# Kernel optimization log

Measured on AMD Instinct MI355X. Metric: run time of the kernel, lower is better.

The kernel has to match this reference:

```python
import jax, jax.numpy as jnp
import numpy as np

B, T, C, H = 16, 512, 1080, 20  # batch, seq, embd, heads; head_dim = C // H = 54

def setup_inputs() -> dict:
    key = jax.random.key(0)
    k1, k2, k3, k4, k5 = jax.random.split(key, 5)
    s = 0.02
    return {
        "x": jax.random.normal(k1, (B, T, C), dtype=jnp.float32),
        "W_attn": jax.random.normal(k2, (C, 3 * C), dtype=jnp.float32) * s,
        "b_attn": jax.random.normal(k3, (3 * C,), dtype=jnp.float32) * s,
        "W_proj": jax.random.normal(k4, (C, C), dtype=jnp.float32) * s,
        "b_proj": jax.random.normal(k5, (C,), dtype=jnp.float32) * s,
    }

def reference(x, W_attn, b_attn, W_proj, b_proj):
    Bb, Tt, Cc = x.shape
    hd = Cc // H
    qkv = jnp.einsum('btc,cd->btd', x, W_attn) + b_attn  # [B,T,3C]
    q, k, v = jnp.split(qkv, 3, axis=2)
    # [B,T,C] -> [B,H,T,hd]
    q = q.reshape(Bb, Tt, H, hd).transpose(0, 2, 1, 3)
    k = k.reshape(Bb, Tt, H, hd).transpose(0, 2, 1, 3)
    v = v.reshape(Bb, Tt, H, hd).transpose(0, 2, 1, 3)
    att = jnp.einsum('bhqd,bhkd->bhqk', q, k) * (1.0 / jnp.sqrt(jnp.float32(hd)))
    causal = jnp.tril(jnp.ones((Tt, Tt), dtype=bool))
    att = jnp.where(causal, att, -jnp.inf)
    att = jax.nn.softmax(att, axis=-1)
    y = jnp.einsum('bhqk,bhkd->bhqd', att, v)  # [B,H,T,hd]
    y = y.transpose(0, 2, 1, 3).reshape(Bb, Tt, Cc)
    return jnp.einsum('btc,cd->btd', y, W_proj) + b_proj
```

## Files before the change

### kernel.cpp

```cpp
#include <hip/hip_runtime.h>
#include <hip/hip_bf16.h>

#define B_   16
#define T_   512
#define C_   1080
#define H_   20
#define HD_  54
#define DP_  64
#define M_   (B_ * T_)
#define KP_  1088
#define NT_  17
#define NQKV_ 3840
#define NPRJ_ 1152
#define NBT_ (B_ * H_ * T_)

typedef short bf16x8 __attribute__((ext_vector_type(8)));
typedef float f32x4  __attribute__((ext_vector_type(4)));
typedef unsigned short u16x8 __attribute__((ext_vector_type(8)));

__device__ __forceinline__ void gload_lds16(const void* g, void* l) {
    __builtin_amdgcn_global_load_lds(
        (const __attribute__((address_space(1))) void*)g,
        (__attribute__((address_space(3))) void*)l,
        16, 0, 0);
}

__device__ __forceinline__ unsigned short f2b(float x) {
    return __builtin_bit_cast(unsigned short, __float2bfloat16(x));
}

#define PB_CVT  8704
#define PB_WTA  4080
#define PB_WTP  1224
__global__ __launch_bounds__(256) void prep_all(
    const float* __restrict__ x, const float* __restrict__ W_attn,
    const float* __restrict__ W_proj, const float* __restrict__ b_attn,
    __hip_bfloat16* __restrict__ xb,
    __hip_bfloat16* __restrict__ wta, __hip_bfloat16* __restrict__ wtp,
    float* __restrict__ bp)
{
    __shared__ float tile[32][33];
    int id = blockIdx.x;

    if (id < PB_CVT) {
        int idx = id * 256 + threadIdx.x;
        int m = idx / (KP_ / 4), c = idx - m * (KP_ / 4);
        ushort4 o;
        if (c < C_ / 4) {
            float4 v = *reinterpret_cast<const float4*>(x + (size_t)m * C_ + c * 4);
            o.x = f2b(v.x); o.y = f2b(v.y); o.z = f2b(v.z); o.w = f2b(v.w);
        } else {
            o.x = o.y = o.z = o.w = 0;
        }
        *reinterpret_cast<ushort4*>(reinterpret_cast<unsigned short*>(xb) +
                                    (size_t)m * KP_ + c * 4) = o;
        return;
    }
    id -= PB_CVT;
    const int tx = threadIdx.x & 31, ty = threadIdx.x >> 5;

    if (id < PB_WTA) {
        int bx = id % 120, by = id / 120;
        int n0 = bx * 32, k0 = by * 32;
        int np = n0 + tx;
        int which = np / 1280;
        int rem = np - which * 1280;
        int h = rem >> 6, d = rem & 63;
        int sn = which * C_ + h * HD_ + d;
        bool valid = d < HD_;
        #pragma unroll
        for (int i = 0; i < 32; i += 8) {
            int k = k0 + ty + i;
            tile[ty + i][tx] = (valid && k < C_) ? W_attn[(size_t)k * (3 * C_) + sn] : 0.f;
        }
        __syncthreads();
        #pragma unroll
        for (int i = 0; i < 32; i += 8) {
            int n = n0 + ty + i, k = k0 + tx;
            wta[(size_t)n * KP_ + k] = __float2bfloat16(tile[tx][ty + i]);
        }
        return;
    }
    id -= PB_WTA;

    if (id < PB_WTP) {
        int bx = id % 36, by = id / 36;
        int n0 = bx * 32, k0 = by * 32;
        #pragma unroll
        for (int i = 0; i < 32; i += 8) {
            int k = k0 + ty + i, n = n0 + tx;
            tile[ty + i][tx] = (k < C_ && n < C_) ? W_proj[(size_t)k * C_ + n] : 0.f;
        }
        __syncthreads();
        #pragma unroll
        for (int i = 0; i < 32; i += 8) {
            int n = n0 + ty + i, k = k0 + tx;
            wtp[(size_t)n * KP_ + k] = __float2bfloat16(tile[tx][ty + i]);
        }
        return;
    }
    id -= PB_WTP;

    {
        int i = id * 256 + threadIdx.x;
        if (i < NQKV_) {
            int which = i / 1280, rem = i - which * 1280;
            int h = rem >> 6, d = rem & 63;
            float v = (d < HD_) ? b_attn[which * C_ + h * HD_ + d] : 0.f;
            if (which == 2 && d == 63) v = 1.0f;
            bp[i] = v;
        }
    }
}

#define BAR_() __builtin_amdgcn_s_barrier()
#define LGKM0_() do { asm volatile("s_waitcnt lgkmcnt(0)" ::: "memory"); \
                      __builtin_amdgcn_sched_barrier(0); } while (0)
#define MFMA_QUAD(Q) do { __builtin_amdgcn_s_setprio(1);                      \
    _Pragma("unroll") for (int kk = 0; kk < 2; ++kk)                          \
    _Pragma("unroll") for (int i = 0; i < 2; ++i)                             \
    _Pragma("unroll") for (int ni = 0; ni < 4; ++ni)                          \
        acc[(Q) * 2 + i][ni] = __builtin_amdgcn_mfma_f32_16x16x32_bf16(       \
            af[kk][i], bfr[ni][kk], acc[(Q) * 2 + i][ni], 0, 0, 0);           \
    __builtin_amdgcn_s_setprio(0); } while (0)

__global__ __launch_bounds__(512, 2) void gemm256(
    const unsigned short* __restrict__ A,
    const unsigned short* __restrict__ Bt,
    const float* __restrict__ bias,
    unsigned short* __restrict__ outQ,
    unsigned short* __restrict__ outK,
    unsigned short* __restrict__ outV)
{
    __shared__ __align__(16) char smem[131072];

    const int tid  = threadIdx.x;
    const int lane = tid & 63;
    const int wv   = tid >> 6;
    const int wr   = wv >> 2;
    const int wc   = wv & 3;
    const int lq   = lane & 15;
    const int lg   = lane >> 4;

    const int id  = blockIdx.y * 15 + blockIdx.x;
    const int xcd = id & 7;
    const int j   = id >> 3;
    const int m0  = (xcd * 4 + (j & 3)) * 256;
    const int n0  = (j >> 2) * 256;

    unsigned gA[2], gB[2];
    const int ld0 = tid * 16, ld1 = tid * 16 + 8192;
    #pragma unroll
    for (int i = 0; i < 2; ++i) {
        int ci = tid + i * 512;
        int r  = ci >> 3;
        int kc = (ci & 7) ^ (r & 7);
        gA[i] = (unsigned)(m0 + r) * KP_ + kc * 8;
        gB[i] = (unsigned)(n0 + r) * KP_ + kc * 8;
    }
    const unsigned HALFSTEP = 128u * KP_;

    auto stage = [&](int buf, int hIdx, unsigned k0) {
        char* sb = smem + buf * 65536 +
                   (hIdx < 2 ? hIdx * 16384 : 32768 + (hIdx - 2) * 16384);
        const unsigned short* sp = (hIdx < 2) ? A : Bt;
        unsigned extra = (hIdx & 1) ? HALFSTEP : 0u;
        gload_lds16(sp + ((hIdx < 2) ? gA[0] : gB[0]) + extra + k0, sb + ld0);
        gload_lds16(sp + ((hIdx < 2) ? gA[1] : gB[1]) + extra + k0, sb + ld1);
    };

    const int s0 = (lg ^ (lq & 7)) * 16;
    const int s1 = ((4 + lg) ^ (lq & 7)) * 16;
    const int aBase = wr * 16384 + lq * 128;
    const int bBase = 32768 + (wc >> 1) * 16384 + (wc & 1) * 8192 + lq * 128;

    auto readA = [&](const char* Ab, int q, bf16x8 (&af)[2][2]) {
        #pragma unroll
        for (int i = 0; i < 2; ++i) {
            af[0][i] = *reinterpret_cast<const bf16x8*>(Ab + (q * 2 + i) * 2048 + s0);
            af[1][i] = *reinterpret_cast<const bf16x8*>(Ab + (q * 2 + i) * 2048 + s1);
        }
    };
    auto readB = [&](const char* Bb, bf16x8 (&bfr)[4][2]) {
        #pragma unroll
        for (int ni = 0; ni < 4; ++ni) {
            bfr[ni][0] = *reinterpret_cast<const bf16x8*>(Bb + ni * 2048 + s0);
            bfr[ni][1] = *reinterpret_cast<const bf16x8*>(Bb + ni * 2048 + s1);
        }
    };

    f32x4 acc[8][4] = {};

    stage(0, 2, 0); stage(0, 3, 0);
    stage(0, 0, 0); stage(0, 1, 0);
    stage(1, 2, 64); stage(1, 3, 64);
    asm volatile("s_waitcnt vmcnt(4)" ::: "memory");
    BAR_();

    const char* Ab0 = smem + aBase;
    const char* Bb0 = smem + bBase;
    const char* Ab1 = smem + 65536 + aBase;
    const char* Bb1 = smem + 65536 + bBase;

    for (int it = 0; it < 8; ++it) {
        const unsigned kT1 = (unsigned)(2 * it + 1) * 64;
        const unsigned kT2 = (unsigned)(2 * it + 2) * 64;
        const unsigned kT3 = (unsigned)(2 * it + 3) * 64;
        const bool lastIt = (it == 7);
        bf16x8 bfr[4][2], af[2][2];

        readB(Bb0, bfr); readA(Ab0, 0, af);
        stage(1, 0, kT1); stage(1, 1, kT1);
        BAR_(); LGKM0_(); MFMA_QUAD(0); BAR_();
        readA(Ab0, 1, af);
        stage(0, 2, kT2);
        BAR_(); LGKM0_(); MFMA_QUAD(1); BAR_();
        readA(Ab0, 2, af);
        stage(0, 3, kT2);
        BAR_(); LGKM0_(); MFMA_QUAD(2); BAR_();
        readA(Ab0, 3, af);
        asm volatile("s_waitcnt vmcnt(4)" ::: "memory");
        BAR_(); LGKM0_(); MFMA_QUAD(3); BAR_();
        readB(Bb1, bfr); readA(Ab1, 0, af);
        stage(0, 0, kT2); stage(0, 1, kT2);
        BAR_(); LGKM0_(); MFMA_QUAD(0); BAR_();
        readA(Ab1, 1, af);
        if (!lastIt) stage(1, 2, kT3);
        BAR_(); LGKM0_(); MFMA_QUAD(1); BAR_();
        readA(Ab1, 2, af);
        if (!lastIt) stage(1, 3, kT3);
        BAR_(); LGKM0_(); MFMA_QUAD(2); BAR_();
        readA(Ab1, 3, af);
        if (!lastIt) asm volatile("s_waitcnt vmcnt(4)" ::: "memory");
        else         asm volatile("s_waitcnt vmcnt(0)" ::: "memory");
        BAR_(); LGKM0_(); MFMA_QUAD(3); BAR_();
    }

    {
        bf16x8 bfr[4][2], af[2][2];
        readB(Bb0, bfr);
        readA(Ab0, 0, af); LGKM0_(); MFMA_QUAD(0);
        readA(Ab0, 1, af); LGKM0_(); MFMA_QUAD(1);
        readA(Ab0, 2, af); LGKM0_(); MFMA_QUAD(2);
        readA(Ab0, 3, af); LGKM0_(); MFMA_QUAD(3);
    }
    __syncthreads();

    const int which = n0 / 1280;
    if (which < 2) {
        unsigned short* dst = which ? outK : outQ;
        #pragma unroll
        for (int mi = 0; mi < 8; ++mi) {
            int mg = m0 + wr * 128 + mi * 16 + lg * 4;
            int b = mg >> 9, t0 = mg & (T_ - 1);
            #pragma unroll
            for (int ni = 0; ni < 4; ++ni) {
                int nl = wc * 64 + ni * 16 + lq;
                int ng = n0 + nl - which * 1280;
                int h = ng >> 6, d = ng & 63;
                float bs = bias[n0 + nl];
                size_t basei = ((size_t)(b * H_ + h) * T_ + t0) * DP_ + d;
                #pragma unroll
                for (int j2 = 0; j2 < 4; ++j2)
                    dst[basei + (size_t)j2 * DP_] = f2b(acc[mi][ni][j2] + bs);
            }
        }
    } else {
        unsigned short* lt = (unsigned short*)smem;
        #pragma unroll
        for (int hm = 0; hm < 2; ++hm) {
            if (hm == 1) __syncthreads();
            if (wr == hm) {
                #pragma unroll
                for (int mi = 0; mi < 8; ++mi) {
                    int ml = mi * 16 + lg * 4;
                    int mc = ml >> 3, mo = ml & 7;
                    #pragma unroll
                    for (int ni = 0; ni < 4; ++ni) {
                        int nl = wc * 64 + ni * 16 + lq;
                        float bs = bias[n0 + nl];
                        ushort4 pk;
                        pk.x = f2b(acc[mi][ni][0] + bs);
                        pk.y = f2b(acc[mi][ni][1] + bs);
                        pk.z = f2b(acc[mi][ni][2] + bs);
                        pk.w = f2b(acc[mi][ni][3] + bs);
                        int slot = mc ^ ((nl >> 3) & 15);
                        *reinterpret_cast<ushort4*>(lt + nl * 136 + slot * 8 + mo) = pk;
                    }
                }
            }
            __syncthreads();
            #pragma unroll
            for (int it = 0; it < 8; ++it) {
                int idx = it * 512 + tid;
                int c2 = idx >> 4, j2 = idx & 15;
                int slot = j2 ^ ((c2 >> 3) & 15);
                u16x8 v = *reinterpret_cast<const u16x8*>(lt + c2 * 136 + slot * 8);
                int ng = n0 + c2 - 2560;
                int h = ng >> 6, d = ng & 63;
                int mg = m0 + hm * 128 + j2 * 8;
                int b = mg >> 9, t = mg & (T_ - 1);
                *reinterpret_cast<u16x8*>(outV + ((size_t)(b * H_ + h) * DP_ + d) * T_ + t) = v;
            }
        }
    }
}

__global__ __launch_bounds__(256) void gemm_mfma_p(
    const unsigned short* __restrict__ A,
    const unsigned short* __restrict__ Bt,
    const float* __restrict__ bias,
    float* __restrict__ outP)
{
    __shared__ __align__(16) char smem[65536];

    const int tid  = threadIdx.x;
    const int lane = tid & 63;
    const int wv   = tid >> 6;
    const int wm   = (wv >> 1) * 64;
    const int wn   = (wv & 1) * 64;
    const int lr   = lane & 15;
    const int lk   = lane >> 4;

    const int gx  = gridDim.x;
    const int gy  = gridDim.y;
    const int id  = blockIdx.y * gx + blockIdx.x;
    const int xcd = id & 7;
    const int j   = id >> 3;
    const int mpc = gy >> 3;
    const int m0  = (xcd * mpc + j % mpc) * 128;
    const int n0  = (j / mpc) * 128;

    unsigned aOff[4], bOff[4];
    int ciB[4];
    #pragma unroll
    for (int it = 0; it < 4; ++it) {
        int ci = it * 256 + tid;
        int r = ci >> 3, p = ci & 7;
        int kc = p ^ (r & 7);
        aOff[it] = (unsigned)(m0 + r) * KP_ + kc * 8;
        bOff[it] = (unsigned)(n0 + r) * KP_ + kc * 8;
        ciB[it] = ci * 16;
    }
    int aRd[2][4], bRd[2][4];
    #pragma unroll
    for (int kk = 0; kk < 2; ++kk) {
        #pragma unroll
        for (int mi = 0; mi < 4; ++mi) {
            int row = wm + mi * 16 + lr;
            aRd[kk][mi] = row * 128 + ((kk * 4 + lk) ^ (row & 7)) * 16;
            int rowb = wn + mi * 16 + lr;
            bRd[kk][mi] = 16384 + rowb * 128 + ((kk * 4 + lk) ^ (rowb & 7)) * 16;
        }
    }

    f32x4 acc[4][4] = {};

    auto stage = [&](int buf, int kt) {
        const unsigned k0 = kt * 64;
        char* sb = smem + buf * 32768;
        #pragma unroll
        for (int it = 0; it < 4; ++it)
            gload_lds16(A + aOff[it] + k0, sb + ciB[it]);
        #pragma unroll
        for (int it = 0; it < 4; ++it)
            gload_lds16(Bt + bOff[it] + k0, sb + 16384 + ciB[it]);
    };

    stage(0, 0);
    for (int kt = 0; kt < NT_; ++kt) {
        const int c = kt & 1;
        if (kt + 1 < NT_) {
            stage(1 - c, kt + 1);
            asm volatile("s_waitcnt vmcnt(8)" ::: "memory");
        } else {
            asm volatile("s_waitcnt vmcnt(0)" ::: "memory");
        }
        __builtin_amdgcn_s_barrier();
        asm volatile("" ::: "memory");

        const char* base = smem + c * 32768;
        #pragma unroll
        for (int kk = 0; kk < 2; ++kk) {
            bf16x8 af[4], bfr[4];
            #pragma unroll
            for (int mi = 0; mi < 4; ++mi)
                af[mi] = *reinterpret_cast<const bf16x8*>(base + aRd[kk][mi]);
            #pragma unroll
            for (int ni = 0; ni < 4; ++ni)
                bfr[ni] = *reinterpret_cast<const bf16x8*>(base + bRd[kk][ni]);
            #pragma unroll
            for (int mi = 0; mi < 4; ++mi)
                #pragma unroll
                for (int ni = 0; ni < 4; ++ni)
                    acc[mi][ni] = __builtin_amdgcn_mfma_f32_16x16x32_bf16(
                        af[mi], bfr[ni], acc[mi][ni], 0, 0, 0);
        }
        asm volatile("" ::: "memory");
        __builtin_amdgcn_s_barrier();
    }

    #pragma unroll
    for (int mi = 0; mi < 4; ++mi) {
        int mrow = m0 + wm + mi * 16 + lk * 4;
        #pragma unroll
        for (int ni = 0; ni < 4; ++ni) {
            int n = n0 + wn + ni * 16 + lr;
            if (n < C_) {
                float bs = bias[n];
                #pragma unroll
                for (int j2 = 0; j2 < 4; ++j2)
                    outP[(size_t)(mrow + j2) * C_ + n] = acc[mi][ni][j2] + bs;
            }
        }
    }
}

__global__ __launch_bounds__(512) void attn_mfma(
    const unsigned short* __restrict__ Q, const unsigned short* __restrict__ K,
    const unsigned short* __restrict__ Vt, __hip_bfloat16* __restrict__ Y)
{
    __shared__ __align__(16) char kvs[16384];
    __shared__ __align__(16) unsigned short ps[8][16][72];

    const int tid  = threadIdx.x;
    const int lane = tid & 63;
    const int wv   = tid >> 6;
    const int grp  = wv >> 2;
    const int wq   = wv & 3;
    const int lq   = lane & 15;
    const int lg   = lane >> 4;
    const int bh   = blockIdx.y;
    const int qt_own = blockIdx.x * 2 + grp;
    const int qbase  = qt_own * 64;
    const float cs = 0.13608276348795434f * 1.44269504f;

    bf16x8 qf[2];
    {
        const unsigned short* qp = Q + ((size_t)bh * T_ + qbase + wq * 16 + lq) * DP_;
        qf[0] = *reinterpret_cast<const bf16x8*>(qp + lg * 8);
        qf[1] = *reinterpret_cast<const bf16x8*>(qp + 32 + lg * 8);
    }

    const int sr = tid >> 3, sp = tid & 7;
    const int spc = sp ^ (sr & 7);
    const unsigned kOff = (unsigned)(sr * DP_ + spc * 8);
    const unsigned vOff = (unsigned)(sr * T_ + spc * 8);
    const unsigned short* Kb = K  + (size_t)bh * T_ * DP_;
    const unsigned short* Vb = Vt + (size_t)bh * DP_ * T_;

    f32x4 o[4] = {};
    unsigned short* pbase = &ps[wv][0][0];
    const int nt = blockIdx.x * 2 + 2;

    for (int kt = 0; kt < nt; ++kt) {
        const int kbase = kt * 64;
        gload_lds16(Kb + kOff + (unsigned)kbase * DP_, kvs + tid * 16);
        gload_lds16(Vb + vOff + (unsigned)kbase, kvs + 8192 + tid * 16);
        __syncthreads();

        if (kt <= qt_own) {
            f32x4 s[4] = {};
            __builtin_amdgcn_s_setprio(1);
            #pragma unroll
            for (int dc = 0; dc < 2; ++dc) {
                #pragma unroll
                for (int ni = 0; ni < 4; ++ni) {
                    int row = ni * 16 + lq;
                    int ch  = (dc * 4 + lg) ^ (row & 7);
                    bf16x8 kf = *reinterpret_cast<const bf16x8*>(kvs + row * 128 + ch * 16);
                    s[ni] = __builtin_amdgcn_mfma_f32_16x16x32_bf16(qf[dc], kf, s[ni], 0, 0, 0);
                }
            }
            __builtin_amdgcn_s_setprio(0);

            if (kt == qt_own) {
                #pragma unroll
                for (int ni = 0; ni < 4; ++ni) {
                    int kg = kbase + ni * 16 + lq;
                    #pragma unroll
                    for (int j = 0; j < 4; ++j) {
                        int qg = qbase + wq * 16 + lg * 4 + j;
                        s[ni][j] = (kg > qg) ? -3.0e38f : s[ni][j];
                    }
                }
            }
            #pragma unroll
            for (int ni = 0; ni < 4; ++ni) {
                #pragma unroll
                for (int j = 0; j < 4; ++j) {
                    float p = exp2f(s[ni][j] * cs);
                    int qr = lg * 4 + j;
                    int cidx = (ni * 2 + (lq >> 3)) ^ (qr & 7);
                    pbase[qr * 72 + cidx * 8 + (lq & 7)] = f2b(p);
                }
            }

            asm volatile("s_waitcnt lgkmcnt(0)" ::: "memory");
            __builtin_amdgcn_sched_barrier(0);

            __builtin_amdgcn_s_setprio(1);
            #pragma unroll
            for (int dc = 0; dc < 2; ++dc) {
                int cc = (dc * 4 + lg) ^ (lq & 7);
                bf16x8 pf = *reinterpret_cast<const bf16x8*>(pbase + lq * 72 + cc * 8);
                #pragma unroll
                for (int ni = 0; ni < 4; ++ni) {
                    int row = ni * 16 + lq;
                    int ch  = (dc * 4 + lg) ^ (row & 7);
                    bf16x8 vf = *reinterpret_cast<const bf16x8*>(kvs + 8192 + row * 128 + ch * 16);
                    o[ni] = __builtin_amdgcn_mfma_f32_16x16x32_bf16(pf, vf, o[ni], 0, 0, 0);
                }
            }
            __builtin_amdgcn_s_setprio(0);
        }
        __syncthreads();
    }

    const int b = bh / H_, h = bh - b * H_;
    #pragma unroll
    for (int j = 0; j < 4; ++j) {
        float l = __shfl(o[3][j], (lane & 48) | 15, 64);
        float inv = 1.f / l;
        int t = qbase + wq * 16 + lg * 4 + j;
        #pragma unroll
        for (int ni = 0; ni < 4; ++ni) {
            int d = ni * 16 + lq;
            if (d < HD_)
                Y[((size_t)b * T_ + t) * KP_ + h * HD_ + d] =
                    __float2bfloat16(o[ni][j] * inv);
        }
    }
}

extern "C" void kernel_launch(void* const* d_in, const int* in_sizes, int n_in,
                              void* d_out, int out_size, void* d_ws, size_t ws_size,
                              hipStream_t stream)
{
    const float* x      = (const float*)d_in[0];
    const float* W_attn = (const float*)d_in[1];
    const float* b_attn = (const float*)d_in[2];
    const float* W_proj = (const float*)d_in[3];
    const float* b_proj = (const float*)d_in[4];
    float* out = (float*)d_out;

    __hip_bfloat16* xb = (__hip_bfloat16*)d_ws;
    unsigned short* qb = (unsigned short*)(xb + (size_t)M_ * KP_);
    unsigned short* kb = qb + (size_t)NBT_ * DP_;
    unsigned short* vtb = kb + (size_t)NBT_ * DP_;
    __hip_bfloat16* wta = (__hip_bfloat16*)(vtb + (size_t)NBT_ * DP_);
    __hip_bfloat16* wtp = wta + (size_t)NQKV_ * KP_;
    float* bp = (float*)(wtp + (size_t)NPRJ_ * KP_);
    __hip_bfloat16* yb = xb;

    prep_all<<<PB_CVT + PB_WTA + PB_WTP + 15, 256, 0, stream>>>(
        x, W_attn, W_proj, b_attn, xb, wta, wtp, bp);

    gemm256<<<dim3(NQKV_ / 256, M_ / 256), 512, 0, stream>>>(
        (const unsigned short*)xb, (const unsigned short*)wta, bp,
        qb, kb, vtb);

    attn_mfma<<<dim3(T_ / 128, B_ * H_), 512, 0, stream>>>(qb, kb, vtb, yb);

    gemm_mfma_p<<<dim3(NPRJ_ / 128, M_ / 128), 256, 0, stream>>>(
        (const unsigned short*)yb, (const unsigned short*)wtp, b_proj, out);
}
```

Measured before the change: 163.0 us.

## Restructure projection GEMM into fine-grained half-tile staged pipeline with prioritized MFMA quads

Rewrites the output-projection GEMM main loop to stage A/B tiles in 64-row halves interleaved with per-quadrant MFMA groups, using barriers, lgkmcnt waits and setprio around each MFMA burst, mirroring the scheme used in the QKV GEMM. It also sets launch bounds to two blocks per CU and hardcodes the grid mapping (9 columns, 8 M-tiles per XCD). The aim is to overlap global-to-LDS loads with MFMA work at finer granularity and raise occupancy. In exchange it adds many barriers per k-step and hardcodes grid dimensions, which breaks if the launch shape changes.

```diff
diff --git a/kernel.cpp b/kernel.cpp
--- a/kernel.cpp
+++ b/kernel.cpp
@@ -122,6 +122,12 @@
     _Pragma("unroll") for (int ni = 0; ni < 4; ++ni)                          \
         acc[(Q) * 2 + i][ni] = __builtin_amdgcn_mfma_f32_16x16x32_bf16(       \
             af[kk][i], bfr[ni][kk], acc[(Q) * 2 + i][ni], 0, 0, 0);           \
+    __builtin_amdgcn_s_setprio(0); } while (0)
+#define MFMA_QUAD_P(Q) do { __builtin_amdgcn_s_setprio(1);                    \
+    _Pragma("unroll") for (int kk = 0; kk < 2; ++kk)                          \
+    _Pragma("unroll") for (int ni = 0; ni < 4; ++ni)                          \
+        acc[(Q)][ni] = __builtin_amdgcn_mfma_f32_16x16x32_bf16(               \
+            af[kk], bfr[ni][kk], acc[(Q)][ni], 0, 0, 0);                      \
     __builtin_amdgcn_s_setprio(0); } while (0)
 
 __global__ __launch_bounds__(512, 2) void gemm256(
@@ -306,7 +312,7 @@
     }
 }
 
-__global__ __launch_bounds__(256) void gemm_mfma_p(
+__global__ __launch_bounds__(256, 2) void gemm_mfma_p(
     const unsigned short* __restrict__ A,
     const unsigned short* __restrict__ Bt,
     const float* __restrict__ bias,
@@ -317,95 +323,117 @@
     const int tid  = threadIdx.x;
     const int lane = tid & 63;
     const int wv   = tid >> 6;
-    const int wm   = (wv >> 1) * 64;
-    const int wn   = (wv & 1) * 64;
-    const int lr   = lane & 15;
-    const int lk   = lane >> 4;
-
-    const int gx  = gridDim.x;
-    const int gy  = gridDim.y;
-    const int id  = blockIdx.y * gx + blockIdx.x;
+    const int wr   = wv >> 1;
+    const int wc   = wv & 1;
+    const int lq   = lane & 15;
+    const int lg   = lane >> 4;
+
+    const int id  = blockIdx.y * 9 + blockIdx.x;
     const int xcd = id & 7;
     const int j   = id >> 3;
-    const int mpc = gy >> 3;
-    const int m0  = (xcd * mpc + j % mpc) * 128;
-    const int n0  = (j / mpc) * 128;
-
-    unsigned aOff[4], bOff[4];
-    int ciB[4];
+    const int m0  = (xcd * 8 + (j & 7)) * 128;
+    const int n0  = (j >> 3) * 128;
+
+    unsigned gA[2], gB[2];
+    const int ld0 = tid * 16, ld1 = tid * 16 + 4096;
     #pragma unroll
-    for (int it = 0; it < 4; ++it) {
-        int ci = it * 256 + tid;
-        int r = ci >> 3, p = ci & 7;
-        int kc = p ^ (r & 7);
-        aOff[it] = (unsigned)(m0 + r) * KP_ + kc * 8;
-        bOff[it] = (unsigned)(n0 + r) * KP_ + kc * 8;
-        ciB[it] = ci * 16;
-    }
-    int aRd[2][4], bRd[2][4];
-    #pragma unroll
-    for (int kk = 0; kk < 2; ++kk) {
-        #pragma unroll
-        for (int mi = 0; mi < 4; ++mi) {
-            int row = wm + mi * 16 + lr;
-            aRd[kk][mi] = row * 128 + ((kk * 4 + lk) ^ (row & 7)) * 16;
-            int rowb = wn + mi * 16 + lr;
-            bRd[kk][mi] = 16384 + rowb * 128 + ((kk * 4 + lk) ^ (rowb & 7)) * 16;
-        }
-    }
+    for (int i = 0; i < 2; ++i) {
+        int ci = tid + i * 256;
+        int r  = ci >> 3;
+        int kc = (ci & 7) ^ (r & 7);
+        gA[i] = (unsigned)(m0 + r) * KP_ + kc * 8;
+        gB[i] = (unsigned)(n0 + r) * KP_ + kc * 8;
+    }
+    const unsigned HALFSTEP = 64u * KP_;
+
+    auto stage = [&](int buf, int hIdx, unsigned k0) {
+        char* sb = smem + buf * 32768 +
+                   (hIdx < 2 ? hIdx * 8192 : 16384 + (hIdx - 2) * 8192);
+        const unsigned short* sp = (hIdx < 2) ? A : Bt;
+        unsigned extra = (hIdx & 1) ? HALFSTEP : 0u;
+        gload_lds16(sp + ((hIdx < 2) ? gA[0] : gB[0]) + extra + k0, sb + ld0);
+        gload_lds16(sp + ((hIdx < 2) ? gA[1] : gB[1]) + extra + k0, sb + ld1);
+    };
+
+    const int s0 = (lg ^ (lq & 7)) * 16;
+    const int s1 = ((4 + lg) ^ (lq & 7)) * 16;
+    const int aBase = wr * 8192 + lq * 128;
+    const int bBase = 16384 + wc * 8192 + lq * 128;
+
+    auto readA = [&](const char* Ab, int q, bf16x8 (&af)[2]) {
+        af[0] = *reinterpret_cast<const bf16x8*>(Ab + q * 2048 + s0);
+        af[1] = *reinterpret_cast<const bf16x8*>(Ab + q * 2048 + s1);
+    };
+    auto readB = [&](const char* Bb, bf16x8 (&bfr)[4][2]) {
+        #pragma unroll
+        for (int ni = 0; ni < 4; ++ni) {
+            bfr[ni][0] = *reinterpret_cast<const bf16x8*>(Bb + ni * 2048 + s0);
+            bfr[ni][1] = *reinterpret_cast<const bf16x8*>(Bb + ni * 2048 + s1);
+        }
+    };
 
     f32x4 acc[4][4] = {};
 
-    auto stage = [&](int buf, int kt) {
-        const unsigned k0 = kt * 64;
-        char* sb = smem + buf * 32768;
-        #pragma unroll
-        for (int it = 0; it < 4; ++it)
-            gload_lds16(A + aOff[it] + k0, sb + ciB[it]);
-        #pragma unroll
-        for (int it = 0; it < 4; ++it)
-            gload_lds16(Bt + bOff[it] + k0, sb + 16384 + ciB[it]);
-    };
-
-    stage(0, 0);
-    for (int kt = 0; kt < NT_; ++kt) {
-        const int c = kt & 1;
-        if (kt + 1 < NT_) {
-            stage(1 - c, kt + 1);
-            asm volatile("s_waitcnt vmcnt(8)" ::: "memory");
-        } else {
-            asm volatile("s_waitcnt vmcnt(0)" ::: "memory");
-        }
-        __builtin_amdgcn_s_barrier();
-        asm volatile("" ::: "memory");
-
-        const char* base = smem + c * 32768;
-        #pragma unroll
-        for (int kk = 0; kk < 2; ++kk) {
-            bf16x8 af[4], bfr[4];
-            #pragma unroll
-            for (int mi = 0; mi < 4; ++mi)
-                af[mi] = *reinterpret_cast<const bf16x8*>(base + aRd[kk][mi]);
-            #pragma unroll
-            for (int ni = 0; ni < 4; ++ni)
-                bfr[ni] = *reinterpret_cast<const bf16x8*>(base + bRd[kk][ni]);
-            #pragma unroll
-            for (int mi = 0; mi < 4; ++mi)
-                #pragma unroll
-                for (int ni = 0; ni < 4; ++ni)
-                    acc[mi][ni] = __builtin_amdgcn_mfma_f32_16x16x32_bf16(
-                        af[mi], bfr[ni], acc[mi][ni], 0, 0, 0);
-        }
-        asm volatile("" ::: "memory");
-        __builtin_amdgcn_s_barrier();
+    stage(0, 2, 0); stage(0, 3, 0);
+    stage(0, 0, 0); stage(0, 1, 0);
+    stage(1, 2, 64); stage(1, 3, 64);
+    asm volatile("s_waitcnt vmcnt(4)" ::: "memory");
+    BAR_();
+
+    const char* Ab0 = smem + aBase;
+    const char* Bb0 = smem + bBase;
+    const char* Ab1 = smem + 32768 + aBase;
+    const char* Bb1 = smem + 32768 + bBase;
+
+    for (int it = 0; it < 8; ++it) {
+        const unsigned kT1 = (unsigned)(2 * it + 1) * 64;
+        const unsigned kT2 = (unsigned)(2 * it + 2) * 64;
+        const unsigned kT3 = (unsigned)(2 * it + 3) * 64;
+        const bool lastIt = (it == 7);
+        bf16x8 bfr[4][2], af[2];
+
+        readB(Bb0, bfr); readA(Ab0, 0, af);
+        stage(1, 0, kT1); stage(1, 1, kT1);
+        BAR_(); LGKM0_(); MFMA_QUAD_P(0); BAR_();
+        readA(Ab0, 1, af);
+        stage(0, 2, kT2);
+        BAR_(); LGKM0_(); MFMA_QUAD_P(1); BAR_();
+        readA(Ab0, 2, af);
+        stage(0, 3, kT2);
+        BAR_(); LGKM0_(); MFMA_QUAD_P(2); BAR_();
+        readA(Ab0, 3, af);
+        asm volatile("s_waitcnt vmcnt(4)" ::: "memory");
+        BAR_(); LGKM0_(); MFMA_QUAD_P(3); BAR_();
+        readB(Bb1, bfr); readA(Ab1, 0, af);
+        stage(0, 0, kT2); stage(0, 1, kT2);
+        BAR_(); LGKM0_(); MFMA_QUAD_P(0); BAR_();
+        readA(Ab1, 1, af);
+        if (!lastIt) stage(1, 2, kT3);
+        BAR_(); LGKM0_(); MFMA_QUAD_P(1); BAR_();
+        readA(Ab1, 2, af);
+        if (!lastIt) stage(1, 3, kT3);
+        BAR_(); LGKM0_(); MFMA_QUAD_P(2); BAR_();
+        readA(Ab1, 3, af);
+        if (!lastIt) asm volatile("s_waitcnt vmcnt(4)" ::: "memory");
+        else         asm volatile("s_waitcnt vmcnt(0)" ::: "memory");
+        BAR_(); LGKM0_(); MFMA_QUAD_P(3); BAR_();
+    }
+
+    {
+        bf16x8 bfr[4][2], af[2];
+        readB(Bb0, bfr);
+        readA(Ab0, 0, af); LGKM0_(); MFMA_QUAD_P(0);
+        readA(Ab0, 1, af); LGKM0_(); MFMA_QUAD_P(1);
+        readA(Ab0, 2, af); LGKM0_(); MFMA_QUAD_P(2);
+        readA(Ab0, 3, af); LGKM0_(); MFMA_QUAD_P(3);
     }
 
     #pragma unroll
     for (int mi = 0; mi < 4; ++mi) {
-        int mrow = m0 + wm + mi * 16 + lk * 4;
+        int mrow = m0 + wr * 64 + mi * 16 + lg * 4;
         #pragma unroll
         for (int ni = 0; ni < 4; ++ni) {
-            int n = n0 + wn + ni * 16 + lr;
+            int n = n0 + wc * 64 + ni * 16 + lq;
             if (n < C_) {
                 float bs = bias[n];
                 #pragma unroll
```

Result: faster. 159.6 us (-2.1%).
